# Optimization experiments

Measured on AMD Instinct MI355X. Metric: run time of the kernel, lower is better.

Reference implementation:

```python
import jax, jax.numpy as jnp
import numpy as np

HID, HEADS, DH, L, OUT = 128, 8, 16, 2, 64
NQ, NA, E, IN = 50000, 50000, 400000, 128
SCALE = float(1.0 / np.sqrt(DH))


def _seg_softmax(alpha, dst, n):
    # softmax over incoming edges of each destination node
    amax = jax.ops.segment_max(alpha, dst, num_segments=n)
    ex = jnp.exp(alpha - amax[dst])
    den = jax.ops.segment_sum(ex, dst, num_segments=n)
    return ex / den[dst]


def _msg(k_src, v_src, q_dst, ei, ar, mr, pr, n_dst):
    # HGTConv message passing for one edge type.
    src, dst = ei[0], ei[1]
    ke = jnp.einsum('ehd,hdf->ehf', k_src[src], ar)  # relation-specific key transform [E,H,DH]
    ve = jnp.einsum('ehd,hdf->ehf', v_src[src], mr)  # relation-specific value transform [E,H,DH]
    alpha = (q_dst[dst] * ke).sum(-1) * pr * SCALE   # [E,H]
    attn = _seg_softmax(alpha, dst, n_dst)
    return jax.ops.segment_sum(attn[..., None] * ve, dst, num_segments=n_dst)  # [n_dst,H,DH]


def setup_inputs():
    key = jax.random.key(0)
    ks = jax.random.split(key, 24)
    f = lambda k, shp: jax.random.normal(k, shp, jnp.float32) * 0.05
    zb = lambda shp: jnp.zeros(shp, jnp.float32)
    return dict(
        x_q=jax.random.normal(ks[0], (NQ, IN), jnp.float32),
        x_a=jax.random.normal(ks[1], (NA, IN), jnp.float32),
        lin0_wq=f(ks[2], (IN, HID)), lin0_bq=zb((HID,)),
        lin0_wa=f(ks[3], (IN, HID)), lin0_ba=zb((HID,)),
        kw_q=f(ks[4], (L, HID, HID)), kb_q=zb((L, HID)),
        qw_q=f(ks[5], (L, HID, HID)), qb_q=zb((L, HID)),
        vw_q=f(ks[6], (L, HID, HID)), vb_q=zb((L, HID)),
        aw_q=f(ks[7], (L, HID, HID)), ab_q=zb((L, HID)),
        kw_a=f(ks[8], (L, HID, HID)), kb_a=zb((L, HID)),
        qw_a=f(ks[9], (L, HID, HID)), qb_a=zb((L, HID)),
        vw_a=f(ks[10], (L, HID, HID)), vb_a=zb((L, HID)),
        aw_a=f(ks[11], (L, HID, HID)), ab_a=zb((L, HID)),
        skip_q=jnp.ones((L,), jnp.float32),
        skip_a=jnp.ones((L,), jnp.float32),
        a_rel=f(ks[12], (L, 2, HEADS, DH, DH)) + jnp.eye(DH, dtype=jnp.float32),
        m_rel=f(ks[13], (L, 2, HEADS, DH, DH)) + jnp.eye(DH, dtype=jnp.float32),
        p_rel=jnp.ones((L, 2, HEADS), jnp.float32),
        lin_w=f(ks[14], (HID, OUT)), lin_b=zb((OUT,)),
        ei_qa=jax.random.randint(ks[15], (2, E), 0, NQ),
        ei_aq=jax.random.randint(ks[16], (2, E), 0, NA),
    )


def reference(x_q, x_a, lin0_wq, lin0_bq, lin0_wa, lin0_ba,
              kw_q, kb_q, qw_q, qb_q, vw_q, vb_q, aw_q, ab_q,
              kw_a, kb_a, qw_a, qb_a, vw_a, vb_a, aw_a, ab_a,
              skip_q, skip_a, a_rel, m_rel, p_rel, lin_w, lin_b,
              ei_qa, ei_aq):
    # per-type input projection + relu
    xq = jax.nn.relu(x_q @ lin0_wq + lin0_bq)
    xa = jax.nn.relu(x_a @ lin0_wa + lin0_ba)
    for l in range(L):
        kq = (xq @ kw_q[l] + kb_q[l]).reshape(NQ, HEADS, DH)
        qq = (xq @ qw_q[l] + qb_q[l]).reshape(NQ, HEADS, DH)
        vq = (xq @ vw_q[l] + vb_q[l]).reshape(NQ, HEADS, DH)
        ka = (xa @ kw_a[l] + kb_a[l]).reshape(NA, HEADS, DH)
        qa = (xa @ qw_a[l] + qb_a[l]).reshape(NA, HEADS, DH)
        va = (xa @ vw_a[l] + vb_a[l]).reshape(NA, HEADS, DH)
        # edge type 0: question -> answer ; edge type 1: answer -> question; group='sum'
        out_a = _msg(kq, vq, qa, ei_qa, a_rel[l, 0], m_rel[l, 0], p_rel[l, 0], NA).reshape(NA, HID)
        out_q = _msg(ka, va, qq, ei_aq, a_rel[l, 1], m_rel[l, 1], p_rel[l, 1], NQ).reshape(NQ, HID)
        oq = jax.nn.gelu(out_q, approximate=False) @ aw_q[l] + ab_q[l]
        oa = jax.nn.gelu(out_a, approximate=False) @ aw_a[l] + ab_a[l]
        gq = jax.nn.sigmoid(skip_q[l])
        ga = jax.nn.sigmoid(skip_a[l])
        xq = gq * oq + (1.0 - gq) * xq
        xa = ga * oa + (1.0 - ga) * xa
    zq = xq @ lin_w + lin_b
    za = xa @ lin_w + lin_b
    # z_dict concatenated: rows [0,NQ) = question, [NQ,NQ+NA) = answer
    return jnp.concatenate([zq, za], axis=0)
```

## Files before the change

### kernel.cpp

```cpp
#include <hip/hip_runtime.h>
#include <hip/hip_bf16.h>
#include <math.h>

typedef __attribute__((ext_vector_type(8))) _Float16 half8;
typedef __attribute__((ext_vector_type(4))) float f32x4;
typedef unsigned short u16;
typedef unsigned int u32;

__device__ __forceinline__ u16 f2h(float f) {
    union { _Float16 h; u16 u; } c; c.h = (_Float16)f; return c.u;
}
__device__ __forceinline__ float h2f(u16 u) {
    union { u16 u; _Float16 h; } c; c.u = u; return (float)c.h;
}
__device__ __forceinline__ float bf2f(u16 u) {
    union { u32 i; float f; } x; x.i = ((u32)u) << 16; return x.f;
}
__device__ __forceinline__ u16 f2bf(float f) {
    union { float f; u32 i; } u; u.f = f;
    u32 r = u.i + 0x7fffu + ((u.i >> 16) & 1u);
    return (u16)(r >> 16);
}
__device__ __forceinline__ float dotpair(u32 a, u32 b) {
    union { u32 i; float f; } alo, ahi, blo, bhi;
    alo.i = a << 16; ahi.i = a & 0xffff0000u;
    blo.i = b << 16; bhi.i = b & 0xffff0000u;
    return alo.f * blo.f + ahi.f * bhi.f;
}
__device__ __forceinline__ int swz_idx(int m, int k) {
    return ((((m >> 4) * 4 + (k >> 5)) * 4 + ((k >> 3) & 3)) * 16 + (m & 15)) * 8 + (k & 7);
}

struct TJob { const float* src; u16* hi; u16* lo; int M; };
struct TJobs { TJob j[11]; };

__global__ void prep_wt_all_k(TJobs jobs) {
    TJob t = jobs.j[blockIdx.y];
    int idx = blockIdx.x * 256 + threadIdx.x;
    if (idx >= t.M * 128) return;
    int m = idx >> 7, k = idx & 127;
    float w = t.src[k * t.M + m];
    u16 h = f2h(w);
    int o = swz_idx(m, k);
    t.hi[o] = h;
    t.lo[o] = f2h(w - h2f(h));
}

__global__ void prep_fused_k(const float* kw_q, const float* kw_a,
                             const float* vw_q, const float* vw_a,
                             const float* a_rel, const float* m_rel,
                             u16* WQh, u16* WQl, u16* WAh, u16* WAl) {
    int j = blockIdx.y;
    int l = j >> 2, dir = (j >> 1) & 1, kv = j & 1;
    const float* w = kv ? (dir ? vw_a : vw_q) : (dir ? kw_a : kw_q);
    w += l * 16384;
    const float* rel = (kv ? m_rel : a_rel) + (l * 2 + dir) * 2048;
    u16* dhi = (dir ? WAh : WQh) + (l * 3 + kv) * 16384;
    u16* dlo = (dir ? WAl : WQl) + (l * 3 + kv) * 16384;
    int idx = blockIdx.x * 256 + threadIdx.x;
    int m = idx >> 7, k = idx & 127;
    int h = m >> 4, f = m & 15;
    float s = 0.f;
#pragma unroll
    for (int d = 0; d < 16; d++)
        s += w[k * 128 + h * 16 + d] * rel[(h * 16 + d) * 16 + f];
    u16 hh = f2h(s);
    int o = swz_idx(m, k);
    dhi[o] = hh;
    dlo[o] = f2h(s - h2f(hh));
}

__global__ void prep_bias_k(const float* kb_q, const float* vb_q, const float* qb_q,
                            const float* kb_a, const float* vb_a, const float* qb_a,
                            const float* a_rel, const float* m_rel,
                            float* BQ, float* BA) {
    int idx = blockIdx.x * 256 + threadIdx.x;
    if (idx >= 1536) return;
    int side = idx / 768, r = idx % 768;
    int l = r / 384, m = r % 384;
    float* dst = side ? BA : BQ;
    if (m >= 256) {
        const float* qb = side ? qb_a : qb_q;
        dst[l * 384 + m] = qb[l * 128 + (m - 256)];
        return;
    }
    int kv = m >> 7, mc = m & 127, h = mc >> 4, f = mc & 15;
    const float* b = side ? (kv ? vb_a : kb_a) : (kv ? vb_q : kb_q);
    b += l * 128;
    const float* rel = (kv ? m_rel : a_rel) + (l * 2 + side) * 2048;
    float s = 0.f;
#pragma unroll
    for (int d = 0; d < 16; d++) s += b[h * 16 + d] * rel[(h * 16 + d) * 16 + f];
    dst[l * 384 + m] = s;
}

__global__ void hist2_k(const int* dA, int Ea, int* degA,
                        const int* dB, int Eb, int* degB) {
    int y = blockIdx.y;
    const int* dst = y ? dB : dA; int E = y ? Eb : Ea; int* deg = y ? degB : degA;
    int i = blockIdx.x * 256 + threadIdx.x;
    if (i < E) atomicAdd(&deg[dst[i]], 1);
}
__global__ void scanA2_k(const int* degA, int* inclA, int* bsumA, int nA,
                         const int* degB, int* inclB, int* bsumB, int nB) {
    int y = blockIdx.y;
    const int* deg = y ? degB : degA; int* incl = y ? inclB : inclA;
    int* bsum = y ? bsumB : bsumA; int n = y ? nB : nA;
    __shared__ int s[256];
    int i = blockIdx.x * 256 + threadIdx.x;
    int v = (i < n) ? deg[i] : 0;
    s[threadIdx.x] = v;
    __syncthreads();
    for (int off = 1; off < 256; off <<= 1) {
        int t = (threadIdx.x >= off) ? s[threadIdx.x - off] : 0;
        __syncthreads();
        s[threadIdx.x] += t;
        __syncthreads();
    }
    if (i < n) incl[i] = s[threadIdx.x];
    if (threadIdx.x == 255) bsum[blockIdx.x] = s[255];
}
__global__ void scanB2_k(int* bsumA, int nbA, int* bsumB, int nbB) {
    int* bsum = blockIdx.x ? bsumB : bsumA;
    int nb = blockIdx.x ? nbB : nbA;
    __shared__ int s[256];
    int v = (threadIdx.x < nb) ? bsum[threadIdx.x] : 0;
    s[threadIdx.x] = v;
    __syncthreads();
    for (int off = 1; off < 256; off <<= 1) {
        int t = (threadIdx.x >= off) ? s[threadIdx.x - off] : 0;
        __syncthreads();
        s[threadIdx.x] += t;
        __syncthreads();
    }
    if (threadIdx.x < nb) bsum[threadIdx.x] = s[threadIdx.x] - v;
}
__global__ void scanC2_k(const int* inclA, const int* degA, const int* bsumA,
                         int* offsA, int* curA, int nA, int Ea,
                         const int* inclB, const int* degB, const int* bsumB,
                         int* offsB, int* curB, int nB, int Eb) {
    int y = blockIdx.y;
    const int* incl = y ? inclB : inclA; const int* deg = y ? degB : degA;
    const int* bsum = y ? bsumB : bsumA;
    int* offs = y ? offsB : offsA; int* cur = y ? curB : curA;
    int n = y ? nB : nA; int E = y ? Eb : Ea;
    int i = blockIdx.x * 256 + threadIdx.x;
    if (i < n) {
        int o = incl[i] - deg[i] + bsum[blockIdx.x];
        offs[i] = o;
        cur[i] = o;
    }
    if (i == 0) offs[n] = E;
}
__global__ void scatter2_k(const int* eiA, int Ea, int* curA, int* srccA,
                           const int* eiB, int Eb, int* curB, int* srccB) {
    int y = blockIdx.y;
    const int* ei = y ? eiB : eiA; int E = y ? Eb : Ea;
    int* cur = y ? curB : curA; int* srcc = y ? srccB : srccA;
    int e = blockIdx.x * 256 + threadIdx.x;
    if (e < E) {
        int p = atomicAdd(&cur[ei[E + e]], 1);
        srcc[p] = ei[e];
    }
}

struct EJob {
    const int* offs; const int* srcc;
    const u16* kt; const u16* vt; const u16* qd;
    const float* pr;
    u16* mhi; int n;
};
struct EJobs { EJob j[2]; };

__global__ __launch_bounds__(256) void edge_fused_k(EJobs jobs) {
    EJob J = jobs.j[blockIdx.y];
    int lane = threadIdx.x & 63;
    int node = blockIdx.x * 4 + (threadIdx.x >> 6);
    if (node >= J.n) return;
    int s0 = J.offs[node], s1 = J.offs[node + 1];
    int h = lane & 7, jj = lane >> 3;
    int hc = lane >> 3;

    float accx = 0.f, accy = 0.f, den = 0.f;

    if (s0 < s1) {
        const u16* qrow = J.qd + (size_t)node * 128 + h * 16;
        uint4 q0 = *(const uint4*)qrow;
        uint4 q1 = *(const uint4*)(qrow + 8);
        float prh = J.pr[h] * 0.25f;

        int jf = s0 + jj;
        int src_next = J.srcc[(jf < s1) ? jf : (s1 - 1)];
        for (int base = s0; base < s1; base += 8) {
            int cnt = s1 - base; if (cnt > 8) cnt = 8;
            int src = src_next;
            if (base + 8 < s1) {
                int jn = base + 8 + jj;
                src_next = J.srcc[(jn < s1) ? jn : (s1 - 1)];
            }
            const u16* krow = J.kt + (size_t)src * 128 + h * 16;
            uint4 k0 = *(const uint4*)krow;
            uint4 k1 = *(const uint4*)(krow + 8);
            float a = dotpair(k0.x, q0.x) + dotpair(k0.y, q0.y)
                    + dotpair(k0.z, q0.z) + dotpair(k0.w, q0.w)
                    + dotpair(k1.x, q1.x) + dotpair(k1.y, q1.y)
                    + dotpair(k1.z, q1.z) + dotpair(k1.w, q1.w);
            float p = (jj < cnt) ? __expf(a * prh) : 0.f;
            den += p;

            u32 vv[8];
#pragma unroll
            for (int t = 0; t < 8; t++) {
                int s2 = __shfl(src, t * 8);
                vv[t] = (t < cnt) ? *(const u32*)(J.vt + (size_t)s2 * 128 + lane * 2) : 0u;
            }
#pragma unroll
            for (int t = 0; t < 8; t++) {
                float w = __shfl(p, t * 8 + hc);
                accx += w * bf2f((u16)(vv[t] & 0xffffu));
                accy += w * bf2f((u16)(vv[t] >> 16));
            }
        }
        den += __shfl_xor(den, 8);
        den += __shfl_xor(den, 16);
        den += __shfl_xor(den, 32);
    }

    float dc = __shfl(den, hc);
    float inv = (dc > 0.f) ? (1.f / dc) : 0.f;
    float vx = accx * inv, vy = accy * inv;
    vx = 0.5f * vx * (1.f + erff(vx * 0.70710678118654752f));
    vy = 0.5f * vy * (1.f + erff(vy * 0.70710678118654752f));
    size_t ob = (size_t)node * 128 + lane * 2;
    *(u32*)(J.mhi + ob) = (u32)f2h(vx) | ((u32)f2h(vy) << 16);
}


struct GJob3 { const u16* xhi; const u16* wh; const float* bias;
               u16* y0; u16* y1; u16* y2; int N; };
struct GJobs3 { GJob3 j[2]; };

__global__ __launch_bounds__(256, 3) void gemm_proj3_k(GJobs3 jobs) {
    GJob3 J = jobs.j[blockIdx.y];
    int tid = threadIdx.x;
    int wave = tid >> 6, lane = tid & 63;
    int lr = lane & 15, kg = lane >> 4;
    u16* const ys[3] = {J.y0, J.y1, J.y2};

    half8 wh[3][2][4];
#pragma unroll
    for (int c = 0; c < 3; c++)
#pragma unroll
        for (int ct = 0; ct < 2; ct++)
#pragma unroll
            for (int ks = 0; ks < 4; ks++) {
                int o = c * 16384 + ((wave * 2 + ct) * 4 + ks) * 512 + kg * 128 + lr * 8;
                wh[c][ct][ks] = *(const half8*)(J.wh + o);
            }

    int N = J.N;
    int ntiles = (N + 15) >> 4;
    for (int t = blockIdx.x; t < ntiles; t += gridDim.x) {
        int arow = t * 16 + lr;
        if (arow >= N) arow = N - 1;
        const u16* ph = J.xhi + (size_t)arow * 128 + kg * 8;
        half8 ah[4];
#pragma unroll
        for (int ks = 0; ks < 4; ks++) ah[ks] = *(const half8*)(ph + ks * 32);

        int crow0 = t * 16 + kg * 4;
#pragma unroll
        for (int c = 0; c < 3; c++) {
            f32x4 acc[2] = {f32x4{0.f, 0.f, 0.f, 0.f}, f32x4{0.f, 0.f, 0.f, 0.f}};
#pragma unroll
            for (int ks = 0; ks < 4; ks++)
#pragma unroll
                for (int ct = 0; ct < 2; ct++)
                    acc[ct] = __builtin_amdgcn_mfma_f32_16x16x32_f16(ah[ks], wh[c][ct][ks], acc[ct], 0, 0, 0);
#pragma unroll
            for (int ct = 0; ct < 2; ct++) {
                int col = (wave * 2 + ct) * 16 + lr;
                float bcol = J.bias[c * 128 + col];
#pragma unroll
                for (int r = 0; r < 4; r++) {
                    int gr = crow0 + r;
                    if (gr < N) ys[c][(size_t)gr * 128 + col] = f2bf(acc[ct][r] + bcol);
                }
            }
        }
    }
}

struct SJob { const u16* mhi; const u16* wh; const u16* wl;
              const float* bias; u16* xhi; const float* gate; int N; };
struct SJobs { SJob j[2]; };

__global__ __launch_bounds__(256, 4) void gemm_skip_k(SJobs jobs) {
    SJob J = jobs.j[blockIdx.y];
    int tid = threadIdx.x;
    int wave = tid >> 6, lane = tid & 63;
    int lr = lane & 15, kg = lane >> 4;

    half8 wh[2][4], wl[2][4];
#pragma unroll
    for (int ct = 0; ct < 2; ct++)
#pragma unroll
        for (int ks = 0; ks < 4; ks++) {
            int o = ((wave * 2 + ct) * 4 + ks) * 512 + kg * 128 + lr * 8;
            wh[ct][ks] = *(const half8*)(J.wh + o);
            wl[ct][ks] = *(const half8*)(J.wl + o);
        }
    float gk = J.gate[0];
    float g = 1.f / (1.f + __expf(-gk));
    float gi = 1.f - g;

    int ntiles = (J.N + 15) >> 4;
    for (int t = blockIdx.x; t < ntiles; t += gridDim.x) {
        int arow = t * 16 + lr;
        if (arow >= J.N) arow = J.N - 1;
        const u16* ph = J.mhi + (size_t)arow * 128 + kg * 8;
        half8 ah[4];
#pragma unroll
        for (int ks = 0; ks < 4; ks++) ah[ks] = *(const half8*)(ph + ks * 32);
        f32x4 acc[2] = {f32x4{0.f, 0.f, 0.f, 0.f}, f32x4{0.f, 0.f, 0.f, 0.f}};
#pragma unroll
        for (int ks = 0; ks < 4; ks++)
#pragma unroll
            for (int ct = 0; ct < 2; ct++) {
                acc[ct] = __builtin_amdgcn_mfma_f32_16x16x32_f16(ah[ks], wh[ct][ks], acc[ct], 0, 0, 0);
                acc[ct] = __builtin_amdgcn_mfma_f32_16x16x32_f16(ah[ks], wl[ct][ks], acc[ct], 0, 0, 0);
            }
        int crow0 = t * 16 + kg * 4;
#pragma unroll
        for (int ct = 0; ct < 2; ct++) {
            int col = (wave * 2 + ct) * 16 + lr;
            float bcol = J.bias[col];
#pragma unroll
            for (int r = 0; r < 4; r++) {
                int gr = crow0 + r;
                if (gr < J.N) {
                    size_t si = (size_t)gr * 128 + col;
                    float v = acc[ct][r] + bcol;
                    v = g * v + gi * h2f(J.xhi[si]);
                    J.xhi[si] = f2h(v);
                }
            }
        }
    }
}

struct FJob { const float* x; const u16* wh; const u16* wl; const float* bias;
              u16* yhi; int N; };
struct FJobs { FJob j[2]; };

__global__ __launch_bounds__(256, 3) void gemm_in_k(FJobs jobs) {
    FJob J = jobs.j[blockIdx.y];
    int tid = threadIdx.x;
    int wave = tid >> 6, lane = tid & 63;
    int lr = lane & 15, kg = lane >> 4;

    half8 wh[2][4], wl[2][4];
#pragma unroll
    for (int ct = 0; ct < 2; ct++)
#pragma unroll
        for (int ks = 0; ks < 4; ks++) {
            int o = ((wave * 2 + ct) * 4 + ks) * 512 + kg * 128 + lr * 8;
            wh[ct][ks] = *(const half8*)(J.wh + o);
            wl[ct][ks] = *(const half8*)(J.wl + o);
        }

    int ntiles = (J.N + 15) >> 4;
    for (int t = blockIdx.x; t < ntiles; t += gridDim.x) {
        int arow = t * 16 + lr;
        if (arow >= J.N) arow = J.N - 1;
        const float* p = J.x + (size_t)arow * 128 + kg * 8;
        half8 ahi[4], alo[4];
#pragma unroll
        for (int ks = 0; ks < 4; ks++) {
            float4 v0 = *(const float4*)(p + ks * 32);
            float4 v1 = *(const float4*)(p + ks * 32 + 4);
            float a8[8] = {v0.x, v0.y, v0.z, v0.w, v1.x, v1.y, v1.z, v1.w};
#pragma unroll
            for (int j = 0; j < 8; j++) {
                _Float16 h = (_Float16)a8[j];
                ahi[ks][j] = h;
                alo[ks][j] = (_Float16)(a8[j] - (float)h);
            }
        }
        f32x4 acc[2] = {f32x4{0.f, 0.f, 0.f, 0.f}, f32x4{0.f, 0.f, 0.f, 0.f}};
#pragma unroll
        for (int ks = 0; ks < 4; ks++)
#pragma unroll
            for (int ct = 0; ct < 2; ct++) {
                acc[ct] = __builtin_amdgcn_mfma_f32_16x16x32_f16(ahi[ks], wh[ct][ks], acc[ct], 0, 0, 0);
                acc[ct] = __builtin_amdgcn_mfma_f32_16x16x32_f16(alo[ks], wh[ct][ks], acc[ct], 0, 0, 0);
                acc[ct] = __builtin_amdgcn_mfma_f32_16x16x32_f16(ahi[ks], wl[ct][ks], acc[ct], 0, 0, 0);
            }
        int crow0 = t * 16 + kg * 4;
#pragma unroll
        for (int ct = 0; ct < 2; ct++) {
            int col = (wave * 2 + ct) * 16 + lr;
            float bcol = J.bias[col];
#pragma unroll
            for (int r = 0; r < 4; r++) {
                int gr = crow0 + r;
                if (gr < J.N) {
                    float v = fmaxf(acc[ct][r] + bcol, 0.f);
                    J.yhi[(size_t)gr * 128 + col] = f2h(v);
                }
            }
        }
    }
}

__global__ __launch_bounds__(256, 4) void gemm_fin_k(
    const u16* __restrict__ Xhi,
    const u16* __restrict__ Wh, const u16* __restrict__ Wl,
    const float* __restrict__ bias, float* __restrict__ Y, int N) {
    int tid = threadIdx.x;
    int wave = tid >> 6, lane = tid & 63;
    int lr = lane & 15, kg = lane >> 4;

    half8 wh[4], wl[4];
#pragma unroll
    for (int ks = 0; ks < 4; ks++) {
        int o = (wave * 4 + ks) * 512 + kg * 128 + lr * 8;
        wh[ks] = *(const half8*)(Wh + o);
        wl[ks] = *(const half8*)(Wl + o);
    }

    int ntiles = (N + 15) >> 4;
    for (int t = blockIdx.x; t < ntiles; t += gridDim.x) {
        int arow = t * 16 + lr;
        if (arow >= N) arow = N - 1;
        const u16* ph = Xhi + (size_t)arow * 128 + kg * 8;
        half8 ah[4];
#pragma unroll
        for (int ks = 0; ks < 4; ks++) ah[ks] = *(const half8*)(ph + ks * 32);
        f32x4 acc = f32x4{0.f, 0.f, 0.f, 0.f};
#pragma unroll
        for (int ks = 0; ks < 4; ks++) {
            acc = __builtin_amdgcn_mfma_f32_16x16x32_f16(ah[ks], wh[ks], acc, 0, 0, 0);
            acc = __builtin_amdgcn_mfma_f32_16x16x32_f16(ah[ks], wl[ks], acc, 0, 0, 0);
        }
        int crow0 = t * 16 + kg * 4;
        int col = wave * 16 + lr;
        float bcol = bias[col];
#pragma unroll
        for (int r = 0; r < 4; r++) {
            int gr = crow0 + r;
            if (gr < N) Y[(size_t)gr * 64 + col] = acc[r] + bcol;
        }
    }
}

extern "C" void kernel_launch(void* const* d_in, const int* in_sizes, int n_in,
                              void* d_out, int out_size, void* d_ws, size_t ws_size,
                              hipStream_t stream) {
    const int NQ = in_sizes[0] / 128;
    const int NA = in_sizes[1] / 128;
    const int Eqa = in_sizes[29] / 2;
    const int Eaq = in_sizes[30] / 2;
    const int NM = (NQ > NA) ? NQ : NA;
    const int EM = (Eqa > Eaq) ? Eqa : Eaq;

    const float* x_q     = (const float*)d_in[0];
    const float* x_a     = (const float*)d_in[1];
    const float* lin0_wq = (const float*)d_in[2];
    const float* lin0_bq = (const float*)d_in[3];
    const float* lin0_wa = (const float*)d_in[4];
    const float* lin0_ba = (const float*)d_in[5];
    const float* kw_q = (const float*)d_in[6];
    const float* kb_q = (const float*)d_in[7];
    const float* qw_q = (const float*)d_in[8];
    const float* qb_q = (const float*)d_in[9];
    const float* vw_q = (const float*)d_in[10];
    const float* vb_q = (const float*)d_in[11];
    const float* aw_q = (const float*)d_in[12];
    const float* ab_q = (const float*)d_in[13];
    const float* kw_a = (const float*)d_in[14];
    const float* kb_a = (const float*)d_in[15];
    const float* qw_a = (const float*)d_in[16];
    const float* qb_a = (const float*)d_in[17];
    const float* vw_a = (const float*)d_in[18];
    const float* vb_a = (const float*)d_in[19];
    const float* aw_a = (const float*)d_in[20];
    const float* ab_a = (const float*)d_in[21];
    const float* skip_q = (const float*)d_in[22];
    const float* skip_a = (const float*)d_in[23];
    const float* a_rel = (const float*)d_in[24];
    const float* m_rel = (const float*)d_in[25];
    const float* p_rel = (const float*)d_in[26];
    const float* lin_w = (const float*)d_in[27];
    const float* lin_b = (const float*)d_in[28];
    const int* ei_qa = (const int*)d_in[29];
    const int* ei_aq = (const int*)d_in[30];

    size_t off = 0;
    auto alloc = [&](size_t bytes) -> void* {
        void* p = (char*)d_ws + off;
        off += (bytes + 255) & ~(size_t)255;
        return p;
    };
    u16* xhi = (u16*)alloc((size_t)(NQ + NA) * 128 * 2);
    u16* xq_hi = xhi;
    u16* xa_hi = xhi + (size_t)NQ * 128;
    u16* mq_hi = (u16*)alloc((size_t)NQ * 128 * 2);
    u16* ma_hi = (u16*)alloc((size_t)NA * 128 * 2);
    u16* kt0 = (u16*)alloc((size_t)NM * 128 * 2);
    u16* vt0 = (u16*)alloc((size_t)NM * 128 * 2);
    u16* qdq = (u16*)alloc((size_t)NM * 128 * 2);
    u16* kt1 = (u16*)alloc((size_t)NM * 128 * 2);
    u16* vt1 = (u16*)alloc((size_t)NM * 128 * 2);
    u16* qda = (u16*)alloc((size_t)NM * 128 * 2);
    int* offs_a = (int*)alloc((size_t)(NA + 1) * 4);
    int* offs_q = (int*)alloc((size_t)(NQ + 1) * 4);
    int* srcc_a = (int*)alloc((size_t)Eqa * 4);
    int* srcc_q = (int*)alloc((size_t)Eaq * 4);
    int* deg    = (int*)alloc((size_t)2 * NM * 4);
    int* cursor = (int*)alloc((size_t)2 * NM * 4);
    int* incl   = (int*)alloc((size_t)2 * NM * 4);
    int* bsum   = (int*)alloc(2048);
    u16* W_LIN0Q_h = (u16*)alloc(16384 * 2); u16* W_LIN0Q_l = (u16*)alloc(16384 * 2);
    u16* W_LIN0A_h = (u16*)alloc(16384 * 2); u16* W_LIN0A_l = (u16*)alloc(16384 * 2);
    u16* WQ_h = (u16*)alloc(2 * 3 * 16384 * 2); u16* WQ_l = (u16*)alloc(2 * 3 * 16384 * 2);
    u16* WA_h = (u16*)alloc(2 * 3 * 16384 * 2); u16* WA_l = (u16*)alloc(2 * 3 * 16384 * 2);
    u16* W_AQ_h = (u16*)alloc(2 * 16384 * 2); u16* W_AQ_l = (u16*)alloc(2 * 16384 * 2);
    u16* W_AA_h = (u16*)alloc(2 * 16384 * 2); u16* W_AA_l = (u16*)alloc(2 * 16384 * 2);
    u16* W_LIN_h = (u16*)alloc(8192 * 2);     u16* W_LIN_l = (u16*)alloc(8192 * 2);
    float* BQ = (float*)alloc(2 * 384 * 4);
    float* BA = (float*)alloc(2 * 384 * 4);
    (void)ws_size; (void)n_in; (void)out_size; (void)EM;

    dim3 B(256);

    TJobs tj;
    tj.j[0]  = {lin0_wq, W_LIN0Q_h, W_LIN0Q_l, 128};
    tj.j[1]  = {lin0_wa, W_LIN0A_h, W_LIN0A_l, 128};
    tj.j[2]  = {qw_q,          WQ_h + (0 * 3 + 2) * 16384, WQ_l + (0 * 3 + 2) * 16384, 128};
    tj.j[3]  = {qw_q + 16384,  WQ_h + (1 * 3 + 2) * 16384, WQ_l + (1 * 3 + 2) * 16384, 128};
    tj.j[4]  = {qw_a,          WA_h + (0 * 3 + 2) * 16384, WA_l + (0 * 3 + 2) * 16384, 128};
    tj.j[5]  = {qw_a + 16384,  WA_h + (1 * 3 + 2) * 16384, WA_l + (1 * 3 + 2) * 16384, 128};
    tj.j[6]  = {aw_q,          W_AQ_h,            W_AQ_l,            128};
    tj.j[7]  = {aw_q + 16384,  W_AQ_h + 16384,    W_AQ_l + 16384,    128};
    tj.j[8]  = {aw_a,          W_AA_h,            W_AA_l,            128};
    tj.j[9]  = {aw_a + 16384,  W_AA_h + 16384,    W_AA_l + 16384,    128};
    tj.j[10] = {lin_w,         W_LIN_h,           W_LIN_l,           64};
    prep_wt_all_k<<<dim3(64, 11), B, 0, stream>>>(tj);
    prep_fused_k<<<dim3(64, 8), B, 0, stream>>>(kw_q, kw_a, vw_q, vw_a, a_rel, m_rel,
                                                WQ_h, WQ_l, WA_h, WA_l);
    prep_bias_k<<<dim3(6), B, 0, stream>>>(kb_q, vb_q, qb_q, kb_a, vb_a, qb_a,
                                           a_rel, m_rel, BQ, BA);

    int* degA = deg;        int* degB = deg + NM;
    int* curA = cursor;     int* curB = cursor + NM;
    int* incA = incl;       int* incB = incl + NM;
    int* bsA  = bsum;       int* bsB  = bsum + 256;
    int gEm = (EM + 255) / 256, gNm = (NM + 255) / 256;
    int gNa = (NA + 255) / 256, gNq = (NQ + 255) / 256;
    hipMemsetAsync(deg, 0, (size_t)2 * NM * 4, stream);
    hist2_k<<<dim3(gEm, 2), B, 0, stream>>>(ei_qa + Eqa, Eqa, degA, ei_aq + Eaq, Eaq, degB);
    scanA2_k<<<dim3(gNm, 2), B, 0, stream>>>(degA, incA, bsA, NA, degB, incB, bsB, NQ);
    scanB2_k<<<dim3(2), B, 0, stream>>>(bsA, gNa, bsB, gNq);
    scanC2_k<<<dim3(gNm, 2), B, 0, stream>>>(incA, degA, bsA, offs_a, curA, NA, Eqa,
                                             incB, degB, bsB, offs_q, curB, NQ, Eaq);
    scatter2_k<<<dim3(gEm, 2), B, 0, stream>>>(ei_qa, Eqa, curA, srcc_a,
                                               ei_aq, Eaq, curB, srcc_q);

    {
        FJobs fj;
        fj.j[0] = {x_q, W_LIN0Q_h, W_LIN0Q_l, lin0_bq, xq_hi, NQ};
        fj.j[1] = {x_a, W_LIN0A_h, W_LIN0A_l, lin0_ba, xa_hi, NA};
        gemm_in_k<<<dim3(512, 2), B, 0, stream>>>(fj);
    }

    for (int l = 0; l < 2; l++) {
        GJobs3 gj;
        gj.j[0] = {xq_hi, WQ_h + l * 3 * 16384, BQ + l * 384, kt0, vt0, qdq, NQ};
        gj.j[1] = {xa_hi, WA_h + l * 3 * 16384, BA + l * 384, kt1, vt1, qda, NA};
        gemm_proj3_k<<<dim3(512, 2), B, 0, stream>>>(gj);

        EJobs ej;
        ej.j[0] = {offs_a, srcc_a, kt0, vt0, qda, p_rel + (l * 2 + 0) * 8, ma_hi, NA};
        ej.j[1] = {offs_q, srcc_q, kt1, vt1, qdq, p_rel + (l * 2 + 1) * 8, mq_hi, NQ};
        edge_fused_k<<<dim3((NM + 3) / 4, 2), B, 0, stream>>>(ej);

        SJobs sj;
        sj.j[0] = {mq_hi, W_AQ_h + l * 16384, W_AQ_l + l * 16384, ab_q + l * 128,
                   xq_hi, skip_q + l, NQ};
        sj.j[1] = {ma_hi, W_AA_h + l * 16384, W_AA_l + l * 16384, ab_a + l * 128,
                   xa_hi, skip_a + l, NA};
        gemm_skip_k<<<dim3(512, 2), B, 0, stream>>>(sj);
    }

    gemm_fin_k<<<dim3(1024, 1), B, 0, stream>>>(
        xhi, W_LIN_h, W_LIN_l, lin_b, (float*)d_out, NQ + NA);
}
```

Before: 409.0 us.

## Fold last-layer skip GEMM and output projection into one precomputed GEMM

Precomputes g*aw[1]@lin_w and (1-g)*lin_w, plus a combined bias, in a small prep kernel. The final layer's skip GEMM and the separate output GEMM are replaced by one kernel that reads both the messages and the layer input and accumulates both products into 64 outputs. This removes one 128x128 GEMM pass and the write and reread of the intermediate hidden state. In exchange, the final kernel does two 128-deep products per row, and the composed weights are rounded differently (hi/lo fp16 split).

```diff
diff --git a/kernel.cpp b/kernel.cpp
--- a/kernel.cpp
+++ b/kernel.cpp
@@ -32,7 +32,7 @@
 }
 
 struct TJob { const float* src; u16* hi; u16* lo; int M; };
-struct TJobs { TJob j[11]; };
+struct TJobs { TJob j[10]; };
 
 __global__ void prep_wt_all_k(TJobs jobs) {
     TJob t = jobs.j[blockIdx.y];
@@ -94,6 +94,38 @@
     dst[l * 384 + m] = s;
 }
 
+__global__ void prep_out_k(const float* aw_q, const float* ab_q, const float* skip_q,
+                           const float* aw_a, const float* ab_a, const float* skip_a,
+                           const float* lin_w, const float* lin_b,
+                           u16* W1h, u16* W1l, u16* W2h, u16* W2l, float* bO) {
+    int side = blockIdx.y;
+    const float* aw = (side ? aw_a : aw_q) + 16384;
+    const float* ab = (side ? ab_a : ab_q) + 128;
+    float gk = (side ? skip_a : skip_q)[1];
+    float g = 1.f / (1.f + __expf(-gk));
+    int idx = blockIdx.x * 256 + threadIdx.x;
+    if (idx >= 8192) return;
+    int k = idx >> 6, m = idx & 63;
+    float s = 0.f;
+#pragma unroll 4
+    for (int d = 0; d < 128; d++) s += aw[k * 128 + d] * lin_w[d * 64 + m];
+    s *= g;
+    int o = swz_idx(m, k);
+    u16 hh = f2h(s);
+    W1h[side * 8192 + o] = hh;
+    W1l[side * 8192 + o] = f2h(s - h2f(hh));
+    float w2 = (1.f - g) * lin_w[k * 64 + m];
+    u16 h2v = f2h(w2);
+    W2h[side * 8192 + o] = h2v;
+    W2l[side * 8192 + o] = f2h(w2 - h2f(h2v));
+    if (k == 0) {
+        float b = 0.f;
+#pragma unroll 4
+        for (int d = 0; d < 128; d++) b += ab[d] * lin_w[d * 64 + m];
+        bO[side * 64 + m] = g * b + lin_b[m];
+    }
+}
+
 __global__ void hist2_k(const int* dA, int Ea, int* degA,
                         const int* dB, int Eb, int* degB) {
     int y = blockIdx.y;
@@ -413,43 +445,55 @@
     }
 }
 
-__global__ __launch_bounds__(256, 4) void gemm_fin_k(
-    const u16* __restrict__ Xhi,
-    const u16* __restrict__ Wh, const u16* __restrict__ Wl,
-    const float* __restrict__ bias, float* __restrict__ Y, int N) {
+struct OJob { const u16* mhi; const u16* xhi;
+              const u16* w1h; const u16* w1l; const u16* w2h; const u16* w2l;
+              const float* bO; float* out; int N; };
+struct OJobs { OJob j[2]; };
+
+__global__ __launch_bounds__(256, 4) void gemm_out_k(OJobs jobs) {
+    OJob J = jobs.j[blockIdx.y];
     int tid = threadIdx.x;
     int wave = tid >> 6, lane = tid & 63;
     int lr = lane & 15, kg = lane >> 4;
 
-    half8 wh[4], wl[4];
+    half8 w1h[4], w1l[4], w2h[4], w2l[4];
 #pragma unroll
     for (int ks = 0; ks < 4; ks++) {
         int o = (wave * 4 + ks) * 512 + kg * 128 + lr * 8;
-        wh[ks] = *(const half8*)(Wh + o);
-        wl[ks] = *(const half8*)(Wl + o);
-    }
-
+        w1h[ks] = *(const half8*)(J.w1h + o);
+        w1l[ks] = *(const half8*)(J.w1l + o);
+        w2h[ks] = *(const half8*)(J.w2h + o);
+        w2l[ks] = *(const half8*)(J.w2l + o);
+    }
+
+    int N = J.N;
     int ntiles = (N + 15) >> 4;
     for (int t = blockIdx.x; t < ntiles; t += gridDim.x) {
         int arow = t * 16 + lr;
         if (arow >= N) arow = N - 1;
-        const u16* ph = Xhi + (size_t)arow * 128 + kg * 8;
-        half8 ah[4];
-#pragma unroll
-        for (int ks = 0; ks < 4; ks++) ah[ks] = *(const half8*)(ph + ks * 32);
+        const u16* pm = J.mhi + (size_t)arow * 128 + kg * 8;
+        const u16* px = J.xhi + (size_t)arow * 128 + kg * 8;
+        half8 am[4], ax[4];
+#pragma unroll
+        for (int ks = 0; ks < 4; ks++) {
+            am[ks] = *(const half8*)(pm + ks * 32);
+            ax[ks] = *(const half8*)(px + ks * 32);
+        }
         f32x4 acc = f32x4{0.f, 0.f, 0.f, 0.f};
 #pragma unroll
         for (int ks = 0; ks < 4; ks++) {
-            acc = __builtin_amdgcn_mfma_f32_16x16x32_f16(ah[ks], wh[ks], acc, 0, 0, 0);
-            acc = __builtin_amdgcn_mfma_f32_16x16x32_f16(ah[ks], wl[ks], acc, 0, 0, 0);
+            acc = __builtin_amdgcn_mfma_f32_16x16x32_f16(am[ks], w1h[ks], acc, 0, 0, 0);
+            acc = __builtin_amdgcn_mfma_f32_16x16x32_f16(am[ks], w1l[ks], acc, 0, 0, 0);
+            acc = __builtin_amdgcn_mfma_f32_16x16x32_f16(ax[ks], w2h[ks], acc, 0, 0, 0);
+            acc = __builtin_amdgcn_mfma_f32_16x16x32_f16(ax[ks], w2l[ks], acc, 0, 0, 0);
         }
         int crow0 = t * 16 + kg * 4;
         int col = wave * 16 + lr;
-        float bcol = bias[col];
+        float bcol = J.bO[col];
 #pragma unroll
         for (int r = 0; r < 4; r++) {
             int gr = crow0 + r;
-            if (gr < N) Y[(size_t)gr * 64 + col] = acc[r] + bcol;
+            if (gr < N) J.out[(size_t)gr * 64 + col] = acc[r] + bcol;
         }
     }
 }
@@ -527,7 +571,9 @@
     u16* WA_h = (u16*)alloc(2 * 3 * 16384 * 2); u16* WA_l = (u16*)alloc(2 * 3 * 16384 * 2);
     u16* W_AQ_h = (u16*)alloc(2 * 16384 * 2); u16* W_AQ_l = (u16*)alloc(2 * 16384 * 2);
     u16* W_AA_h = (u16*)alloc(2 * 16384 * 2); u16* W_AA_l = (u16*)alloc(2 * 16384 * 2);
-    u16* W_LIN_h = (u16*)alloc(8192 * 2);     u16* W_LIN_l = (u16*)alloc(8192 * 2);
+    u16* W1h = (u16*)alloc(2 * 8192 * 2); u16* W1l = (u16*)alloc(2 * 8192 * 2);
+    u16* W2h = (u16*)alloc(2 * 8192 * 2); u16* W2l = (u16*)alloc(2 * 8192 * 2);
+    float* bO = (float*)alloc(2 * 64 * 4);
     float* BQ = (float*)alloc(2 * 384 * 4);
     float* BA = (float*)alloc(2 * 384 * 4);
     (void)ws_size; (void)n_in; (void)out_size; (void)EM;
@@ -545,12 +591,13 @@
     tj.j[7]  = {aw_q + 16384,  W_AQ_h + 16384,    W_AQ_l + 16384,    128};
     tj.j[8]  = {aw_a,          W_AA_h,            W_AA_l,            128};
     tj.j[9]  = {aw_a + 16384,  W_AA_h + 16384,    W_AA_l + 16384,    128};
-    tj.j[10] = {lin_w,         W_LIN_h,           W_LIN_l,           64};
-    prep_wt_all_k<<<dim3(64, 11), B, 0, stream>>>(tj);
+    prep_wt_all_k<<<dim3(64, 10), B, 0, stream>>>(tj);
     prep_fused_k<<<dim3(64, 8), B, 0, stream>>>(kw_q, kw_a, vw_q, vw_a, a_rel, m_rel,
                                                 WQ_h, WQ_l, WA_h, WA_l);
     prep_bias_k<<<dim3(6), B, 0, stream>>>(kb_q, vb_q, qb_q, kb_a, vb_a, qb_a,
                                            a_rel, m_rel, BQ, BA);
+    prep_out_k<<<dim3(32, 2), B, 0, stream>>>(aw_q, ab_q, skip_q, aw_a, ab_a, skip_a,
+                                              lin_w, lin_b, W1h, W1l, W2h, W2l, bO);
 
     int* degA = deg;        int* degB = deg + NM;
     int* curA = cursor;     int* curB = cursor + NM;
@@ -585,14 +632,18 @@
         ej.j[1] = {offs_q, srcc_q, kt1, vt1, qdq, p_rel + (l * 2 + 1) * 8, mq_hi, NQ};
         edge_fused_k<<<dim3((NM + 3) / 4, 2), B, 0, stream>>>(ej);
 
-        SJobs sj;
-        sj.j[0] = {mq_hi, W_AQ_h + l * 16384, W_AQ_l + l * 16384, ab_q + l * 128,
-                   xq_hi, skip_q + l, NQ};
-        sj.j[1] = {ma_hi, W_AA_h + l * 16384, W_AA_l + l * 16384, ab_a + l * 128,
-                   xa_hi, skip_a + l, NA};
-        gemm_skip_k<<<dim3(512, 2), B, 0, stream>>>(sj);
-    }
-
-    gemm_fin_k<<<dim3(1024, 1), B, 0, stream>>>(
-        xhi, W_LIN_h, W_LIN_l, lin_b, (float*)d_out, NQ + NA);
-}
+        if (l == 0) {
+            SJobs sj;
+            sj.j[0] = {mq_hi, W_AQ_h, W_AQ_l, ab_q, xq_hi, skip_q, NQ};
+            sj.j[1] = {ma_hi, W_AA_h, W_AA_l, ab_a, xa_hi, skip_a, NA};
+            gemm_skip_k<<<dim3(512, 2), B, 0, stream>>>(sj);
+        } else {
+            OJobs oj;
+            oj.j[0] = {mq_hi, xq_hi, W1h, W1l, W2h, W2l, bO,
+                       (float*)d_out, NQ};
+            oj.j[1] = {ma_hi, xa_hi, W1h + 8192, W1l + 8192, W2h + 8192, W2l + 8192, bO + 64,
+                       (float*)d_out + (size_t)NQ * 64, NA};
+            gemm_out_k<<<dim3(512, 2), B, 0, stream>>>(oj);
+        }
+    }
+}
```

Measured after the change: 414.0 us. About the same (+1.2%).
